# Optimization experiments

Hardware: AMD Instinct MI355X
Metric: run time of the kernel (lower is better)

Reference implementation:

```python
import jax, jax.numpy as jnp
import numpy as np

N_NODES = 5000
K_POOL = 30
BN_EPS = 1e-5


def setup_inputs() -> dict:
    key = jax.random.key(0)
    ks = jax.random.split(key, 16)
    B, N, Din, C, H, OUT, E = 32, N_NODES, 16, 64, 128, 2, 80000
    F_tot = Din + 3 * C  # concat of input + 3 conv layers = 208
    return {
        "x": jax.random.normal(ks[0], (B, N, Din), jnp.float32),
        "age": jax.random.uniform(ks[1], (B,), jnp.float32) * 100.0,
        "edge_attr": jax.random.uniform(ks[2], (E,), jnp.float32) + 0.1,
        "W0": jax.random.normal(ks[3], (Din, C), jnp.float32) * 0.1,
        "b0": jnp.zeros((C,), jnp.float32),
        "W1": jax.random.normal(ks[4], (C, C), jnp.float32) * 0.1,
        "b1": jnp.zeros((C,), jnp.float32),
        "W2": jax.random.normal(ks[5], (C, C), jnp.float32) * 0.1,
        "b2": jnp.zeros((C,), jnp.float32),
        "g0": jnp.ones((C,), jnp.float32),
        "be0": jnp.zeros((C,), jnp.float32),
        "g1": jnp.ones((C,), jnp.float32),
        "be1": jnp.zeros((C,), jnp.float32),
        "mW0": jax.random.normal(ks[6], (K_POOL * F_tot + 1, H), jnp.float32) * 0.02,
        "mb0": jnp.zeros((H,), jnp.float32),
        "mW1": jax.random.normal(ks[7], (H, OUT), jnp.float32) * 0.1,
        "mb1": jnp.zeros((OUT,), jnp.float32),
        "edge_row": jax.random.randint(ks[8], (E,), 0, N, jnp.int32),
        "edge_col": jax.random.randint(ks[9], (E,), 0, N, jnp.int32),
    }


def _spmm(xw, rows, cols, nv):
    # xw: (B, N, C); out[b, r] = sum_{edges (r,c)} nv * xw[b, c]
    def one(xb):
        return jax.ops.segment_sum(xb[cols] * nv[:, None], rows, num_segments=N_NODES)
    return jax.vmap(one)(xw)


def reference(x, age, edge_attr, W0, b0, W1, b1, W2, b2, g0, be0, g1, be1,
              mW0, mb0, mW1, mb1, edge_row, edge_col):
    N = N_NODES
    # GCN normalization on A + I (gcn_norm with edge weights, self-loop value 1)
    loop = jnp.arange(N, dtype=edge_row.dtype)
    rows = jnp.concatenate([edge_row, loop])
    cols = jnp.concatenate([edge_col, loop])
    vals = jnp.concatenate([edge_attr, jnp.ones((N,), edge_attr.dtype)])
    deg = jax.ops.segment_sum(vals, rows, num_segments=N)
    dinv = jnp.where(deg > 0, jax.lax.rsqrt(jnp.maximum(deg, 1e-12)), 0.0)
    nv = dinv[rows] * vals * dinv[cols]

    feats = [x]
    h = x
    convs = [(W0, b0), (W1, b1), (W2, b2)]
    bns = [(g0, be0), (g1, be1)]
    for i, (W, b) in enumerate(convs):
        h = _spmm(h @ W, rows, cols, nv) + b  # GCNConv
        if i < len(convs) - 1:
            g, be = bns[i]
            mu = jnp.mean(h, axis=(0, 1))   # BatchNorm1d over flattened (B*N, C)
            var = jnp.var(h, axis=(0, 1))
            h = (h - mu) * jax.lax.rsqrt(var + BN_EPS) * g + be
        h = jax.nn.relu(h)  # dropout p=0.0 -> identity
        feats.append(h)

    z = jnp.concatenate(feats, axis=-1)  # (B, N, 208)
    # global_sort_pool: sort nodes by last feature channel, descending, take top-k
    order = jnp.argsort(-z[:, :, -1], axis=1)[:, :K_POOL]  # (B, k)
    zk = jnp.take_along_axis(z, order[:, :, None], axis=1)  # (B, k, 208)
    flat = zk.reshape(z.shape[0], -1)
    flat = jnp.concatenate([flat, age[:, None]], axis=1)  # append age scalar

    hm = jax.nn.relu(flat @ mW0 + mb0)  # MLP head
    out = hm @ mW1 + mb1
    return jax.nn.log_softmax(out, axis=-1)
```

## Files before the change

kernel.cpp:

```cpp
#include <hip/hip_runtime.h>
#include <math.h>

#define NN    5000
#define NE    80000
#define NB    32
#define DIN   16
#define CH    64
#define KPOOL 30
#define FTOT  208
#define FLATW 6241
#define NH    128
#define NG    8
#define GB    4
#define NPB   16
#define NEPAD (NE + 4 * NN)
#define NSLOT 32



__global__ void k_init(float* deg, int* counts, float* stats, float* hm) {
    int i = blockIdx.x * 256 + threadIdx.x;
    if (i < NN) { deg[i] = 1.0f; counts[i] = 0; }
    if (i < 2 * NSLOT * 128) stats[i] = 0.0f;
    if (i < 4096) hm[i] = 0.0f;
}

#define NEB 313
__global__ void k_edgetr(const float* __restrict__ attr, const int* __restrict__ erow,
                         float* deg, int* counts,
                         const float* __restrict__ x, float* __restrict__ xt) {
    if (blockIdx.x < NEB) {
        int e = blockIdx.x * 256 + threadIdx.x;
        if (e < NE) {
            int r = erow[e];
            atomicAdd(&deg[r], attr[e]);
            atomicAdd(&counts[r], 1);
        }
    } else {
        int idx = (blockIdx.x - NEB) * 256 + threadIdx.x;
        if (idx >= NB * NN) return;
        int b = idx / NN, n = idx % NN;
        int g = b >> 2, bi = b & 3;
        const float4* src = (const float4*)(x + (size_t)idx * DIN);
        float4* dst = (float4*)(xt + (((size_t)g * NN + n) * GB + bi) * DIN);
        dst[0] = src[0]; dst[1] = src[1]; dst[2] = src[2]; dst[3] = src[3];
    }
}

__global__ __launch_bounds__(1024) void k_scan(const int* __restrict__ counts,
                                               const float* __restrict__ deg,
                                               int* rowptr, int* cursor, float* dinv) {
    __shared__ int wsum[16], woff[16];
    __shared__ int carry_sh;
    int t = threadIdx.x;
    int lane = t & 63, wid = t >> 6;
    if (t == 0) carry_sh = 0;
    __syncthreads();
    for (int base = 0; base < NN; base += 1024) {
        int carry = carry_sh;
        int i = base + t;
        int v = 0;
        if (i < NN) {
            v = (counts[i] + 3) & ~3;
            dinv[i] = 1.0f / sqrtf(deg[i]);
        }
        int s = v;
#pragma unroll
        for (int off = 1; off < 64; off <<= 1) {
            int o = __shfl_up(s, off);
            if (lane >= off) s += o;
        }
        if (lane == 63) wsum[wid] = s;
        __syncthreads();
        if (t < 16) {
            int w = wsum[t];
#pragma unroll
            for (int off = 1; off < 16; off <<= 1) {
                int o = __shfl_up(w, off);
                if (t >= off) w += o;
            }
            woff[t] = w;
        }
        __syncthreads();
        int inc = s + (wid > 0 ? woff[wid - 1] : 0) + carry;
        if (i < NN) {
            rowptr[i + 1] = inc;
            cursor[i] = inc - v;
        }
        if (t == 1023) carry_sh = carry + woff[15];
        __syncthreads();
    }
    if (t == 0) rowptr[0] = 0;
}

__global__ void k_build(const int* __restrict__ erow, const int* __restrict__ ecol,
                        const float* __restrict__ attr, const float* __restrict__ dinv,
                        const int* __restrict__ counts, const int* __restrict__ rowptr,
                        int* cursor, int* csr_col, float* csr_nv) {
    int t = blockIdx.x * 256 + threadIdx.x;
    if (t < NE) {
        int r = erow[t], c = ecol[t];
        int pos = atomicAdd(&cursor[r], 1);
        csr_col[pos] = c;
        csr_nv[pos] = dinv[r] * attr[t] * dinv[c];
    } else if (t - NE < NN) {
        int i = t - NE;
        int cnt = counts[i];
        int pcnt = (cnt + 3) & ~3;
        int base = rowptr[i + 1] - pcnt;
        for (int p = base + cnt; p < base + pcnt; ++p) { csr_col[p] = i; csr_nv[p] = 0.0f; }
    }
}

template<int ACT>
__device__ __forceinline__ float4 actv(float4 v, float4 s, float4 t) {
    if (ACT) {
        v.x = fmaxf(fmaf(v.x, s.x, t.x), 0.f);
        v.y = fmaxf(fmaf(v.y, s.y, t.y), 0.f);
        v.z = fmaxf(fmaf(v.z, s.z, t.z), 0.f);
        v.w = fmaxf(fmaf(v.w, s.w, t.w), 0.f);
    }
    return v;
}
__device__ __forceinline__ void fma4(float4& a, float w, float4 v) {
    a.x = fmaf(w, v.x, a.x); a.y = fmaf(w, v.y, a.y);
    a.z = fmaf(w, v.z, a.z); a.w = fmaf(w, v.w, a.w);
}

template<int CIN, int ACT, int STATS, int SCORE>
__global__ __launch_bounds__(256) void k_layer(
        const float* __restrict__ in, const float* __restrict__ bnstats,
        const float* __restrict__ gamma, const float* __restrict__ beta,
        const float* __restrict__ W, const float* __restrict__ bias,
        const int* __restrict__ rowptr, const int* __restrict__ csr_col,
        const float* __restrict__ csr_nv, const float* __restrict__ dinv,
        float* __restrict__ out, float* __restrict__ stats,
        float* __restrict__ score) {
    constexpr int ALS = (CIN == 64) ? 68 : 20;
    __shared__ float As[4 * 16 * ALS];
    __shared__ float stl[ACT ? 128 : 4];
    int tid = threadIdx.x;
    int wid = tid >> 6, lane = tid & 63;
    int g = blockIdx.x & 7;
    int nb = (blockIdx.x >> 3) * NPB;
    int base = nb + wid * 4;
    float* Aw = As + wid * 16 * ALS;

    if (ACT) {
        if (tid < 64) {
            float su = 0.f, qu = 0.f;
#pragma unroll
            for (int s = 0; s < NSLOT; ++s) {
                su += bnstats[s * 128 + tid];
                qu += bnstats[s * 128 + 64 + tid];
            }
            const float inv = 1.0f / (float)(NB * NN);
            float mu = su * inv;
            float var = qu * inv - mu * mu;
            float sc = gamma[tid] / sqrtf(var + 1e-5f);
            stl[tid] = sc;
            stl[64 + tid] = fmaf(-mu, sc, beta[tid]);
        }
        __syncthreads();
    }

    if (CIN == 64) {
        const float4* __restrict__ in4 = (const float4*)in + (size_t)g * NN * 64;
        int c4 = lane & 15, bi = lane >> 4;
        float4 sv = {1.f,1.f,1.f,1.f}, tv = {0.f,0.f,0.f,0.f};
        if (ACT) { sv = ((const float4*)stl)[c4]; tv = ((const float4*)(stl + 64))[c4]; }
#pragma unroll
        for (int pr = 0; pr < 2; ++pr) {
            int r0 = base + pr * 2;
            int r1 = r0 + 1;
            bool vn0 = r0 < NN, vn1 = r1 < NN;
            int rc0 = vn0 ? r0 : 0, rc1 = vn1 ? r1 : 0;
            float dd0 = dinv[rc0]; dd0 *= dd0;
            float dd1 = dinv[rc1]; dd1 *= dd1;
            float4 a0 = {0.f,0.f,0.f,0.f}, a1 = {0.f,0.f,0.f,0.f};
            {
                float4 v0 = actv<ACT>(in4[(size_t)rc0 * 64 + lane], sv, tv);
                float4 v1 = actv<ACT>(in4[(size_t)rc1 * 64 + lane], sv, tv);
                if (vn0) { a0.x = dd0 * v0.x; a0.y = dd0 * v0.y; a0.z = dd0 * v0.z; a0.w = dd0 * v0.w; }
                if (vn1) { a1.x = dd1 * v1.x; a1.y = dd1 * v1.y; a1.z = dd1 * v1.z; a1.w = dd1 * v1.w; }
            }
            int p0a = rowptr[rc0], na = vn0 ? (rowptr[rc0 + 1] - p0a) >> 2 : 0;
            int p0b = rowptr[rc1], nbv = vn1 ? (rowptr[rc1 + 1] - p0b) >> 2 : 0;
            int mx = max(na, nbv);
            for (int bb = 0; bb < mx; ++bb) {
                int ea = min(p0a + 4 * bb, NEPAD - 4);
                int eb = min(p0b + 4 * bb, NEPAD - 4);
                bool va = bb < na, vb = bb < nbv;
                int4   ca = *(const int4*)(csr_col + ea);
                float4 wa = *(const float4*)(csr_nv + ea);
                int4   cb = *(const int4*)(csr_col + eb);
                float4 wb = *(const float4*)(csr_nv + eb);
                if (!va) { wa.x = 0.f; wa.y = 0.f; wa.z = 0.f; wa.w = 0.f;
                           ca.x = 0; ca.y = 0; ca.z = 0; ca.w = 0; }
                if (!vb) { wb.x = 0.f; wb.y = 0.f; wb.z = 0.f; wb.w = 0.f;
                           cb.x = 0; cb.y = 0; cb.z = 0; cb.w = 0; }
                float4 u0 = in4[(size_t)ca.x * 64 + lane];
                float4 u1 = in4[(size_t)ca.y * 64 + lane];
                float4 u2 = in4[(size_t)ca.z * 64 + lane];
                float4 u3 = in4[(size_t)ca.w * 64 + lane];
                float4 t0 = in4[(size_t)cb.x * 64 + lane];
                float4 t1 = in4[(size_t)cb.y * 64 + lane];
                float4 t2 = in4[(size_t)cb.z * 64 + lane];
                float4 t3 = in4[(size_t)cb.w * 64 + lane];
                fma4(a0, wa.x, actv<ACT>(u0, sv, tv));
                fma4(a0, wa.y, actv<ACT>(u1, sv, tv));
                fma4(a0, wa.z, actv<ACT>(u2, sv, tv));
                fma4(a0, wa.w, actv<ACT>(u3, sv, tv));
                fma4(a1, wb.x, actv<ACT>(t0, sv, tv));
                fma4(a1, wb.y, actv<ACT>(t1, sv, tv));
                fma4(a1, wb.z, actv<ACT>(t2, sv, tv));
                fma4(a1, wb.w, actv<ACT>(t3, sv, tv));
            }
            *(float4*)(Aw + ((pr * 2 + 0) * 4 + bi) * ALS + c4 * 4) = a0;
            *(float4*)(Aw + ((pr * 2 + 1) * 4 + bi) * ALS + c4 * 4) = a1;
        }
    } else {
        const float* __restrict__ inr = in + (size_t)g * NN * 64;
#pragma unroll
        for (int i = 0; i < 4; ++i) {
            int r = base + i;
            float a = 0.f;
            if (r < NN) {
                float d = dinv[r];
                a = d * d * inr[(size_t)r * 64 + lane];
                int p0 = rowptr[r], p1 = rowptr[r + 1];
                for (int e = p0; e < p1; e += 4) {
                    int4   cc = *(const int4*)(csr_col + e);
                    float4 ww = *(const float4*)(csr_nv + e);
                    float v0 = inr[(size_t)cc.x * 64 + lane];
                    float v1 = inr[(size_t)cc.y * 64 + lane];
                    float v2 = inr[(size_t)cc.z * 64 + lane];
                    float v3 = inr[(size_t)cc.w * 64 + lane];
                    a = fmaf(ww.x, v0, a);
                    a = fmaf(ww.y, v1, a);
                    a = fmaf(ww.z, v2, a);
                    a = fmaf(ww.w, v3, a);
                }
            }
            Aw[(i * 4 + (lane >> 4)) * ALS + (lane & 15)] = a;
        }
    }
    __syncthreads();

    int colq = lane & 15, rowq = lane >> 4;
    int node = base + rowq;

    if (!SCORE) {
        const float4* __restrict__ W4 = (const float4*)W;
        float4 bb = ((const float4*)bias)[colq];
        float4 o[4];
#pragma unroll
        for (int i = 0; i < 4; ++i) o[i] = bb;
#pragma unroll 8
        for (int k = 0; k < CIN; ++k) {
            float4 w4 = W4[k * 16 + colq];
#pragma unroll
            for (int i = 0; i < 4; ++i) {
                float a = Aw[(rowq * 4 + i) * ALS + k];
                fma4(o[i], a, w4);
            }
        }
        if (node < NN) {
            float4* __restrict__ op = (float4*)(out + ((size_t)g * NN + node) * 256);
#pragma unroll
            for (int i = 0; i < 4; ++i) op[i * 16 + colq] = o[i];
        }

        if (STATS) {
            float4 s4 = {0,0,0,0}, q4 = {0,0,0,0};
            if (node < NN) {
#pragma unroll
                for (int i = 0; i < 4; ++i) {
                    s4.x += o[i].x; s4.y += o[i].y; s4.z += o[i].z; s4.w += o[i].w;
                    q4.x = fmaf(o[i].x, o[i].x, q4.x); q4.y = fmaf(o[i].y, o[i].y, q4.y);
                    q4.z = fmaf(o[i].z, o[i].z, q4.z); q4.w = fmaf(o[i].w, o[i].w, q4.w);
                }
            }
            s4.x += __shfl_xor(s4.x, 16); s4.y += __shfl_xor(s4.y, 16);
            s4.z += __shfl_xor(s4.z, 16); s4.w += __shfl_xor(s4.w, 16);
            q4.x += __shfl_xor(q4.x, 16); q4.y += __shfl_xor(q4.y, 16);
            q4.z += __shfl_xor(q4.z, 16); q4.w += __shfl_xor(q4.w, 16);
            s4.x += __shfl_xor(s4.x, 32); s4.y += __shfl_xor(s4.y, 32);
            s4.z += __shfl_xor(s4.z, 32); s4.w += __shfl_xor(s4.w, 32);
            q4.x += __shfl_xor(q4.x, 32); q4.y += __shfl_xor(q4.y, 32);
            q4.z += __shfl_xor(q4.z, 32); q4.w += __shfl_xor(q4.w, 32);
            __syncthreads();
            if (lane < 16) {
                float* S = As + wid * 128;
                *(float4*)(S + lane * 8) = s4;
                *(float4*)(S + lane * 8 + 4) = q4;
            }
            __syncthreads();
            if (tid < 64) {
                int cq = tid >> 2, comp = tid & 3;
                float s = 0.f, q = 0.f;
#pragma unroll
                for (int w = 0; w < 4; ++w) {
                    s += As[w * 128 + cq * 8 + comp];
                    q += As[w * 128 + cq * 8 + 4 + comp];
                }
                float* sl = stats + (blockIdx.x & (NSLOT - 1)) * 128;
                atomicAdd(&sl[tid], s);
                atomicAdd(&sl[64 + tid], q);
            }
        }
    } else {
        if (node < NN) {
            float4* __restrict__ op = (float4*)(out + ((size_t)g * NN + node) * 256);
#pragma unroll
            for (int i = 0; i < 4; ++i)
                op[i * 16 + colq] = *(const float4*)(Aw + (rowq * 4 + i) * ALS + colq * 4);
        }
        if (lane < 16) {
            int nd = base + (lane >> 2);
            if (nd < NN) {
                float s = bias[63];
                const float* Ar = Aw + lane * ALS;
#pragma unroll 8
                for (int k = 0; k < 64; ++k)
                    s = fmaf(Ar[k], W[k * 64 + 63], s);
                score[((size_t)g * NN + nd) * 4 + (lane & 3)] = fmaxf(s, 0.f);
            }
        }
    }
}

__global__ void k_bnfin(const float* __restrict__ stats,
                        const float* __restrict__ g0, const float* __restrict__ be0,
                        const float* __restrict__ g1, const float* __restrict__ be1,
                        float* st) {
    int tid = threadIdx.x;
    int c = tid & 63, layer = tid >> 6;
    const float* sb = stats + layer * NSLOT * 128;
    float su = 0.f, qu = 0.f;
#pragma unroll
    for (int s = 0; s < NSLOT; ++s) {
        su += sb[s * 128 + c];
        qu += sb[s * 128 + 64 + c];
    }
    const float inv = 1.0f / (float)(NB * NN);
    float mu = su * inv;
    float var = qu * inv - mu * mu;
    float g = layer ? g1[c] : g0[c];
    float be = layer ? be1[c] : be0[c];
    float sc = g / sqrtf(var + 1e-5f);
    st[layer * 128 + c] = sc;
    st[layer * 128 + 64 + c] = fmaf(-mu, sc, be);
}

__global__ __launch_bounds__(1024) void k_toppool(const float* __restrict__ sc, int* order) {
    __shared__ unsigned long long wbest[16];
    __shared__ unsigned long long winner;
    int b = blockIdx.x, tid = threadIdx.x;
    int g = b >> 2, bi = b & 3;
    int lane = tid & 63, wid = tid >> 6;
    unsigned long long key[5];
#pragma unroll
    for (int j = 0; j < 5; ++j) {
        int n = tid + j * 1024;
        unsigned long long k = 0;
        if (n < NN) {
            float v = sc[((size_t)g * NN + n) * GB + bi];
            k = ((unsigned long long)__float_as_uint(v) << 32) | (unsigned int)(NN - n);
        }
        key[j] = k;
    }
    for (int k = 0; k < KPOOL; ++k) {
        unsigned long long best = key[0];
#pragma unroll
        for (int j = 1; j < 5; ++j) best = (key[j] > best) ? key[j] : best;
#pragma unroll
        for (int off = 1; off < 64; off <<= 1) {
            unsigned long long o = __shfl_xor(best, off);
            best = (o > best) ? o : best;
        }
        if (lane == 0) wbest[wid] = best;
        __syncthreads();
        if (tid == 0) {
            unsigned long long w = wbest[0];
#pragma unroll
            for (int i = 1; i < 16; ++i) w = (wbest[i] > w) ? wbest[i] : w;
            winner = w;
            order[b * KPOOL + k] = NN - (int)(w & 0xFFFFFFFFu);
        }
        __syncthreads();
        int n = NN - (int)(winner & 0xFFFFFFFFu);
        if ((n & 1023) == tid) key[n >> 10] = 0;
    }
}

__global__ void k_gather(const float* __restrict__ xt, const float* __restrict__ h1,
                         const float* __restrict__ h2, const float* __restrict__ agg,
                         const float* __restrict__ W2, const float* __restrict__ b2,
                         const float* __restrict__ st, const float* __restrict__ age,
                         const int* __restrict__ order, float* __restrict__ flat) {
    int bk = blockIdx.x;
    int b = bk / KPOOL, k = bk % KPOOL;
    int n = order[bk];
    int g = b >> 2, bi = b & 3;
    size_t node = (size_t)g * NN + n;
    int f = threadIdx.x;
    float val = 0.f;
    if (f < DIN) {
        val = xt[(node * GB + bi) * DIN + f];
    } else if (f < DIN + CH) {
        int c = f - DIN;
        val = fmaxf(fmaf(h1[(node * GB + bi) * CH + c], st[c], st[64 + c]), 0.f);
    } else if (f < DIN + 2 * CH) {
        int c = f - DIN - CH;
        val = fmaxf(fmaf(h2[(node * GB + bi) * CH + c], st[128 + c], st[192 + c]), 0.f);
    } else if (f < FTOT) {
        int c = f - DIN - 2 * CH;
        const float* __restrict__ Ar = agg + (node * GB + bi) * CH;
        float s = b2[c];
#pragma unroll 8
        for (int kk = 0; kk < 64; ++kk)
            s = fmaf(Ar[kk], W2[kk * 64 + c], s);
        val = fmaxf(s, 0.f);
    }
    if (f < FTOT) flat[(size_t)b * FLATW + k * FTOT + f] = val;
    if (bk == 0 && f >= FTOT && f < FTOT + NB)
        flat[(size_t)(f - FTOT) * FLATW + (FLATW - 1)] = age[f - FTOT];
}

__global__ void k_head1(const float* __restrict__ flat, const float* __restrict__ mW0,
                        float* hm) {
    int tid = threadIdx.x;
    int j4 = (tid & 31) * 4;
    int b0 = (tid >> 5) * 4;
    int kbase = blockIdx.x * 64;
    float acc[4][4];
#pragma unroll
    for (int i = 0; i < 4; i++)
#pragma unroll
        for (int jj = 0; jj < 4; jj++) acc[i][jj] = 0.f;
    int kend = FLATW - kbase; if (kend > 64) kend = 64;
    for (int kk = 0; kk < kend; ++kk) {
        int k = kbase + kk;
        float4 w = *(const float4*)(mW0 + (size_t)k * NH + j4);
#pragma unroll
        for (int i = 0; i < 4; i++) {
            float fv = flat[(size_t)(b0 + i) * FLATW + k];
            acc[i][0] = fmaf(fv, w.x, acc[i][0]);
            acc[i][1] = fmaf(fv, w.y, acc[i][1]);
            acc[i][2] = fmaf(fv, w.z, acc[i][2]);
            acc[i][3] = fmaf(fv, w.w, acc[i][3]);
        }
    }
#pragma unroll
    for (int i = 0; i < 4; i++)
#pragma unroll
        for (int jj = 0; jj < 4; jj++)
            atomicAdd(&hm[(size_t)(b0 + i) * NH + j4 + jj], acc[i][jj]);
}

__global__ void k_head2(const float* __restrict__ hm, const float* __restrict__ mb0,
                        const float* __restrict__ mW1, const float* __restrict__ mb1,
                        float* __restrict__ out) {
    __shared__ float vals[64];
    int tid = threadIdx.x;
    int b = tid >> 1, o = tid & 1;
    float acc = mb1[o];
    for (int j = 0; j < NH; ++j) {
        float hv = fmaxf(hm[b * NH + j] + mb0[j], 0.f);
        acc = fmaf(hv, mW1[j * 2 + o], acc);
    }
    vals[tid] = acc;
    __syncthreads();
    float v0 = vals[b * 2], v1 = vals[b * 2 + 1];
    float m = fmaxf(v0, v1);
    float lse = m + logf(expf(v0 - m) + expf(v1 - m));
    out[tid] = acc - lse;
}

extern "C" void kernel_launch(void* const* d_in, const int* in_sizes, int n_in,
                              void* d_out, int out_size, void* d_ws, size_t ws_size,
                              hipStream_t stream) {
    const float* x    = (const float*)d_in[0];
    const float* age  = (const float*)d_in[1];
    const float* attr = (const float*)d_in[2];
    const float* W0   = (const float*)d_in[3];
    const float* b0   = (const float*)d_in[4];
    const float* W1   = (const float*)d_in[5];
    const float* b1   = (const float*)d_in[6];
    const float* W2   = (const float*)d_in[7];
    const float* b2   = (const float*)d_in[8];
    const float* g0   = (const float*)d_in[9];
    const float* be0  = (const float*)d_in[10];
    const float* g1   = (const float*)d_in[11];
    const float* be1  = (const float*)d_in[12];
    const float* mW0  = (const float*)d_in[13];
    const float* mb0  = (const float*)d_in[14];
    const float* mW1  = (const float*)d_in[15];
    const float* mb1  = (const float*)d_in[16];
    const int* erow   = (const int*)d_in[17];
    const int* ecol   = (const int*)d_in[18];
    float* out = (float*)d_out;

    float* ws     = (float*)d_ws;
    float* deg    = ws;
    float* dinv   = deg + 5008;
    int*   counts = (int*)(dinv + 5008);
    int*   rowptr = counts + 5008;
    int*   cursor = rowptr + 5008;
    int*   csr_col= cursor + 5008;
    float* csr_nv = (float*)(csr_col + NEPAD);
    float* stats  = csr_nv + NEPAD;
    float* st     = stats + 2 * NSLOT * 128;
    float* sc     = st + 256;
    int*   order  = (int*)(sc + NB * NN);
    float* flat   = (float*)(order + 960);
    float* hm     = flat + (size_t)NB * FLATW;
    float* xt     = hm + 4096;
    float* h1     = xt + (size_t)NB * NN * DIN;
    float* h2     = h1 + (size_t)NB * NN * CH;
    float* agg    = h2 + (size_t)NB * NN * CH;

    k_init<<<32, 256, 0, stream>>>(deg, counts, stats, hm);
    k_edgetr<<<NEB + (NB * NN + 255) / 256, 256, 0, stream>>>(attr, erow, deg, counts, x, xt);
    k_scan<<<1, 1024, 0, stream>>>(counts, deg, rowptr, cursor, dinv);
    k_build<<<(NE + NN + 255) / 256, 256, 0, stream>>>(erow, ecol, attr, dinv, counts, rowptr, cursor, csr_col, csr_nv);

    const int NBLK = ((NN + NPB - 1) / NPB) * NG;
    k_layer<16, 0, 1, 0><<<NBLK, 256, 0, stream>>>(xt, nullptr, nullptr, nullptr, W0, b0, rowptr, csr_col, csr_nv, dinv, h1, stats, nullptr);
    k_layer<64, 1, 1, 0><<<NBLK, 256, 0, stream>>>(h1, stats, g0, be0, W1, b1, rowptr, csr_col, csr_nv, dinv, h2, stats + NSLOT * 128, nullptr);
    k_layer<64, 1, 0, 1><<<NBLK, 256, 0, stream>>>(h2, stats + NSLOT * 128, g1, be1, W2, b2, rowptr, csr_col, csr_nv, dinv, agg, nullptr, sc);

    k_bnfin<<<1, 128, 0, stream>>>(stats, g0, be0, g1, be1, st);
    k_toppool<<<NB, 1024, 0, stream>>>(sc, order);
    k_gather<<<NB * KPOOL, 256, 0, stream>>>(xt, h1, h2, agg, W2, b2, st, age, order, flat);
    k_head1<<<(FLATW + 63) / 64, 256, 0, stream>>>(flat, mW0, hm);
    k_head2<<<1, 64, 0, stream>>>(hm, mb0, mW1, mb1, out);
}
```

Measured before the change: 365.9 us.

## Sort nodes by degree bucket to balance per-wavefront SpMM work

Builds a counting-sort permutation of nodes by padded degree inside the scan kernel and has each layer wavefront process degree-similar nodes via the permutation, reducing divergence from max(na,nb) loops. It also removes a __syncthreads between the aggregation and the transform phase, relying on each wave only using its own shared slice. The cost is scattered node access, which loses locality in input rows and output writes, plus extra serial work in the single-block scan.

```diff
diff --git a/kernel.cpp b/kernel.cpp
--- a/kernel.cpp
+++ b/kernel.cpp
@@ -13,16 +13,18 @@
 #define NG    8
 #define GB    4
 #define NPB   16
+#define NPAD  5008
 #define NEPAD (NE + 4 * NN)
 #define NSLOT 32
 
 
 
-__global__ void k_init(float* deg, int* counts, float* stats, float* hm) {
+__global__ void k_init(float* deg, int* counts, float* stats, float* hm, int* perm) {
     int i = blockIdx.x * 256 + threadIdx.x;
     if (i < NN) { deg[i] = 1.0f; counts[i] = 0; }
     if (i < 2 * NSLOT * 128) stats[i] = 0.0f;
     if (i < 4096) hm[i] = 0.0f;
+    if (i >= NN && i < NPAD) perm[i] = NN;
 }
 
 #define NEB 313
@@ -49,12 +51,15 @@
 
 __global__ __launch_bounds__(1024) void k_scan(const int* __restrict__ counts,
                                                const float* __restrict__ deg,
-                                               int* rowptr, int* cursor, float* dinv) {
+                                               int* rowptr, int* cursor, float* dinv,
+                                               int* perm) {
     __shared__ int wsum[16], woff[16];
     __shared__ int carry_sh;
+    __shared__ int hist[256];
     int t = threadIdx.x;
     int lane = t & 63, wid = t >> 6;
     if (t == 0) carry_sh = 0;
+    if (t < 256) hist[t] = 0;
     __syncthreads();
     for (int base = 0; base < NN; base += 1024) {
         int carry = carry_sh;
@@ -63,6 +68,7 @@
         if (i < NN) {
             v = (counts[i] + 3) & ~3;
             dinv[i] = 1.0f / sqrtf(deg[i]);
+            atomicAdd(&hist[min(v >> 2, 255)], 1);
         }
         int s = v;
 #pragma unroll
@@ -91,6 +97,20 @@
         __syncthreads();
     }
     if (t == 0) rowptr[0] = 0;
+    int mycnt = (t < 256) ? hist[t] : 0;
+    for (int off = 1; off < 256; off <<= 1) {
+        int v = (t < 256 && t >= off) ? hist[t - off] : 0;
+        __syncthreads();
+        if (t < 256) hist[t] += v;
+        __syncthreads();
+    }
+    if (t < 256) hist[t] -= mycnt;
+    __syncthreads();
+    for (int i = t; i < NN; i += 1024) {
+        int b = min(((counts[i] + 3) & ~3) >> 2, 255);
+        int pos = atomicAdd(&hist[b], 1);
+        perm[pos] = i;
+    }
 }
 
 __global__ void k_build(const int* __restrict__ erow, const int* __restrict__ ecol,
@@ -134,6 +154,7 @@
         const float* __restrict__ W, const float* __restrict__ bias,
         const int* __restrict__ rowptr, const int* __restrict__ csr_col,
         const float* __restrict__ csr_nv, const float* __restrict__ dinv,
+        const int* __restrict__ perm,
         float* __restrict__ out, float* __restrict__ stats,
         float* __restrict__ score) {
     constexpr int ALS = (CIN == 64) ? 68 : 20;
@@ -145,6 +166,7 @@
     int nb = (blockIdx.x >> 3) * NPB;
     int base = nb + wid * 4;
     float* Aw = As + wid * 16 * ALS;
+    const int4 pid = *(const int4*)(perm + base);
 
     if (ACT) {
         if (tid < 64) {
@@ -171,10 +193,10 @@
         if (ACT) { sv = ((const float4*)stl)[c4]; tv = ((const float4*)(stl + 64))[c4]; }
 #pragma unroll
         for (int pr = 0; pr < 2; ++pr) {
-            int r0 = base + pr * 2;
-            int r1 = r0 + 1;
-            bool vn0 = r0 < NN, vn1 = r1 < NN;
-            int rc0 = vn0 ? r0 : 0, rc1 = vn1 ? r1 : 0;
+            int id0 = (pr == 0) ? pid.x : pid.z;
+            int id1 = (pr == 0) ? pid.y : pid.w;
+            bool vn0 = id0 < NN, vn1 = id1 < NN;
+            int rc0 = vn0 ? id0 : 0, rc1 = vn1 ? id1 : 0;
             float dd0 = dinv[rc0]; dd0 *= dd0;
             float dd1 = dinv[rc1]; dd1 *= dd1;
             float4 a0 = {0.f,0.f,0.f,0.f}, a1 = {0.f,0.f,0.f,0.f};
@@ -221,9 +243,10 @@
         }
     } else {
         const float* __restrict__ inr = in + (size_t)g * NN * 64;
+        int ids[4] = {pid.x, pid.y, pid.z, pid.w};
 #pragma unroll
         for (int i = 0; i < 4; ++i) {
-            int r = base + i;
+            int r = ids[i];
             float a = 0.f;
             if (r < NN) {
                 float d = dinv[r];
@@ -245,10 +268,9 @@
             Aw[(i * 4 + (lane >> 4)) * ALS + (lane & 15)] = a;
         }
     }
-    __syncthreads();
 
     int colq = lane & 15, rowq = lane >> 4;
-    int node = base + rowq;
+    int node = (rowq == 0) ? pid.x : (rowq == 1) ? pid.y : (rowq == 2) ? pid.z : pid.w;
 
     if (!SCORE) {
         const float4* __restrict__ W4 = (const float4*)W;
@@ -317,7 +339,8 @@
                 op[i * 16 + colq] = *(const float4*)(Aw + (rowq * 4 + i) * ALS + colq * 4);
         }
         if (lane < 16) {
-            int nd = base + (lane >> 2);
+            int q = lane >> 2;
+            int nd = (q == 0) ? pid.x : (q == 1) ? pid.y : (q == 2) ? pid.z : pid.w;
             if (nd < NN) {
                 float s = bias[63];
                 const float* Ar = Aw + lane * ALS;
@@ -508,7 +531,8 @@
     int*   counts = (int*)(dinv + 5008);
     int*   rowptr = counts + 5008;
     int*   cursor = rowptr + 5008;
-    int*   csr_col= cursor + 5008;
+    int*   perm   = cursor + 5008;
+    int*   csr_col= perm + 5008;
     float* csr_nv = (float*)(csr_col + NEPAD);
     float* stats  = csr_nv + NEPAD;
     float* st     = stats + 2 * NSLOT * 128;
@@ -521,15 +545,15 @@
     float* h2     = h1 + (size_t)NB * NN * CH;
     float* agg    = h2 + (size_t)NB * NN * CH;
 
-    k_init<<<32, 256, 0, stream>>>(deg, counts, stats, hm);
+    k_init<<<32, 256, 0, stream>>>(deg, counts, stats, hm, perm);
     k_edgetr<<<NEB + (NB * NN + 255) / 256, 256, 0, stream>>>(attr, erow, deg, counts, x, xt);
-    k_scan<<<1, 1024, 0, stream>>>(counts, deg, rowptr, cursor, dinv);
+    k_scan<<<1, 1024, 0, stream>>>(counts, deg, rowptr, cursor, dinv, perm);
     k_build<<<(NE + NN + 255) / 256, 256, 0, stream>>>(erow, ecol, attr, dinv, counts, rowptr, cursor, csr_col, csr_nv);
 
     const int NBLK = ((NN + NPB - 1) / NPB) * NG;
-    k_layer<16, 0, 1, 0><<<NBLK, 256, 0, stream>>>(xt, nullptr, nullptr, nullptr, W0, b0, rowptr, csr_col, csr_nv, dinv, h1, stats, nullptr);
-    k_layer<64, 1, 1, 0><<<NBLK, 256, 0, stream>>>(h1, stats, g0, be0, W1, b1, rowptr, csr_col, csr_nv, dinv, h2, stats + NSLOT * 128, nullptr);
-    k_layer<64, 1, 0, 1><<<NBLK, 256, 0, stream>>>(h2, stats + NSLOT * 128, g1, be1, W2, b2, rowptr, csr_col, csr_nv, dinv, agg, nullptr, sc);
+    k_layer<16, 0, 1, 0><<<NBLK, 256, 0, stream>>>(xt, nullptr, nullptr, nullptr, W0, b0, rowptr, csr_col, csr_nv, dinv, perm, h1, stats, nullptr);
+    k_layer<64, 1, 1, 0><<<NBLK, 256, 0, stream>>>(h1, stats, g0, be0, W1, b1, rowptr, csr_col, csr_nv, dinv, perm, h2, stats + NSLOT * 128, nullptr);
+    k_layer<64, 1, 0, 1><<<NBLK, 256, 0, stream>>>(h2, stats + NSLOT * 128, g1, be1, W2, b2, rowptr, csr_col, csr_nv, dinv, perm, agg, nullptr, sc);
 
     k_bnfin<<<1, 128, 0, stream>>>(stats, g0, be0, g1, be1, st);
     k_toppool<<<NB, 1024, 0, stream>>>(sc, order);
```

New measurement: 364.8 us. No clear change (-0.3%).
